# Kernel optimization log

Hardware: AMD Instinct MI355X
Metric: run time of the kernel (lower is better)

Reference implementation:

```python
import jax, jax.numpy as jnp
import numpy as np

K = 16  # top-k neighbors (init kwarg k)
EPS = 1e-8


def setup_inputs() -> dict:
    key = jax.random.key(0)
    # bs=8, closeness=12, flows=2, N=2048
    x_c = jax.random.normal(key, (8, 12, 2, 2048), dtype=jnp.float32)
    return {"x_c": x_c, "flow": 0}


def _cosine_adjacency(x):
    # x: (bs, 2, N, closeness) -> per-node feature = concat of both flows over time
    bs, f, N, c = x.shape
    feats = jnp.transpose(x, (0, 2, 1, 3)).reshape(bs, N, f * c)  # (bs, N, 2*closeness)
    fn = feats / (jnp.linalg.norm(feats, axis=-1, keepdims=True) + EPS)
    return jnp.einsum('bnd,bmd->bnm', fn, fn)  # (bs, N, N)


def reference(x_c, flow):
    # x_c: (bs, closeness, 2, N)
    bs, closeness, _, N = x_c.shape
    x = jnp.transpose(x_c, (0, 2, 3, 1)).astype(jnp.float32)  # (bs, 2, N, closeness)

    # mode == 'cos': cosine-similarity adjacency
    A = _cosine_adjacency(x)

    # index = argsort(A, descending)[:, :, :k]  ==  top-k neighbor indices per node
    _, index = jax.lax.top_k(A, K)  # (bs, N, K)

    # batched gather replacing the bs x N python double loop:
    # sx_c[i, j] = x[i, flow, index[i, j]]
    x_flow = x[:, flow]  # (bs, N, closeness)
    sx_c = jax.vmap(lambda xf, idx: xf[idx])(x_flow, index)  # (bs, N, K, closeness)

    # tgt_mode == 'c': tgt = x[:, flow].unsqueeze(-2)  -> (bs, N, 1, closeness)
    tgt = x_flow[:, :, None, :]
    # returned as tgt.permute(0,2,3,1).squeeze(1) -> (bs, closeness, N)
    tgt_out = jnp.squeeze(jnp.transpose(tgt, (0, 2, 3, 1)), axis=1)

    return sx_c, tgt_out
```

## Files before the change

kernel.cpp:

```cpp
#include <hip/hip_runtime.h>
#include <hip/hip_bf16.h>
#include <math.h>

#define BS   8
#define NPTS 2048
#define CCH  12
#define NF   2
#define DIM  24
#define KPAD 32
#define KTOP 16
#define NWV  8
#define RPB  16
#define CBUF 112
#define CBS  113
#define WVS  20

#define NROWS    (BS * NPTS)
#define TGT_BASE (NROWS * KTOP * CCH)

typedef unsigned long long u64;
typedef unsigned int       u32;
typedef unsigned short     u16;
typedef __attribute__((ext_vector_type(8))) short short8;
typedef __attribute__((ext_vector_type(4))) float f32x4;

#define WS_FEATS 0
#define WS_RAW   (NROWS * DIM * 4)
#define WS_FHI   (WS_RAW + NROWS * CCH * 4)
#define WS_FLO   (WS_FHI + NROWS * KPAD * 2)

__device__ __forceinline__ float np_norm_den(const float* __restrict__ v)
{
#pragma clang fp contract(off)
    float s[DIM];
    #pragma unroll
    for (int d = 0; d < DIM; ++d) s[d] = v[d] * v[d];
    float r[8];
    #pragma unroll
    for (int j = 0; j < 8; ++j) r[j] = (s[j] + s[j + 8]) + s[j + 16];
    float res = ((r[0] + r[1]) + (r[2] + r[3])) + ((r[4] + r[5]) + (r[6] + r[7]));
    return sqrtf(res) + 1e-8f;
}

__device__ __forceinline__ u32 ordf(float f)
{
    u32 u = __float_as_uint(f);
    return ((int)u >= 0) ? (u | 0x80000000u) : ~u;
}

__device__ __forceinline__ u16 bf16_rne(float x)
{
    u32 bits = __float_as_uint(x);
    bits += 0x7fffu + ((bits >> 16) & 1u);
    return (u16)(bits >> 16);
}

__global__ __launch_bounds__(64) void prep_kernel(
    const float* __restrict__ x_c,
    const int*   __restrict__ flow_p,
    float*       __restrict__ feats,
    u16*         __restrict__ fhi,
    u16*         __restrict__ flo,
    float*       __restrict__ raw,
    float*       __restrict__ out)
{
    const int t = blockIdx.x * 64 + threadIdx.x;
    const int b = t >> 11;
    const int n = t & (NPTS - 1);
    const float* xb = x_c + (size_t)b * CCH * NF * NPTS;

    float v[DIM];
    float fn[DIM];
    {
#pragma clang fp contract(off)
        #pragma unroll
        for (int c = 0; c < CCH; ++c)
            #pragma unroll
            for (int f = 0; f < NF; ++f)
                v[f * CCH + c] = xb[(c * NF + f) * NPTS + n];

        const float den = np_norm_den(v);
        #pragma unroll
        for (int d = 0; d < DIM; ++d) fn[d] = v[d] / den;
    }

    float* fo = feats + (size_t)t * DIM;
    #pragma unroll
    for (int j = 0; j < 6; ++j)
        *(f32x4*)(fo + 4 * j) = *(f32x4*)(fn + 4 * j);

    u16 hb[KPAD], lb[KPAD];
    #pragma unroll
    for (int d = 0; d < DIM; ++d) {
        const u16 h = bf16_rne(fn[d]);
        const float hf = __uint_as_float((u32)h << 16);
        hb[d] = h;
        lb[d] = bf16_rne(fn[d] - hf);
    }
    #pragma unroll
    for (int d = DIM; d < KPAD; ++d) { hb[d] = 0; lb[d] = 0; }

    u16* ho = fhi + (size_t)t * KPAD;
    u16* lo = flo + (size_t)t * KPAD;
    #pragma unroll
    for (int j = 0; j < 4; ++j) {
        *(short8*)(ho + 8 * j) = ((const short8*)hb)[j];
        *(short8*)(lo + 8 * j) = ((const short8*)lb)[j];
    }

    const int flow = flow_p[0];
    float rv[CCH];
    #pragma unroll
    for (int c = 0; c < CCH; ++c) {
        rv[c] = flow ? v[CCH + c] : v[c];
        out[TGT_BASE + ((size_t)b * CCH + c) * NPTS + n] = rv[c];
    }
    float* ro = raw + (size_t)t * CCH;
    #pragma unroll
    for (int j = 0; j < 3; ++j)
        *(f32x4*)(ro + 4 * j) = *(f32x4*)(rv + 4 * j);
}

#define CLEANUP_DESC(arr)                                         \
    _Pragma("unroll")                                             \
    for (int j_ = 8; j_ > 0; j_ >>= 1)                            \
        _Pragma("unroll")                                         \
        for (int i_ = 0; i_ < KTOP; ++i_) {                       \
            const int l_ = i_ | j_;                               \
            if (l_ > i_) {                                        \
                const float a_ = arr[i_], c_ = arr[l_];           \
                arr[i_] = fmaxf(a_, c_);                          \
                arr[l_] = fminf(a_, c_);                          \
            }                                                     \
        }

#define APPROX_TILE(ACC, AHI, ALO, BHI, BLO)                                  \
    f32x4 ACC  = {0.0f, 0.0f, 0.0f, 0.0f};                                    \
    {                                                                         \
        f32x4 acc2_ = {0.0f, 0.0f, 0.0f, 0.0f};                               \
        ACC   = __builtin_amdgcn_mfma_f32_16x16x32_bf16(AHI, BHI, ACC, 0,0,0);\
        acc2_ = __builtin_amdgcn_mfma_f32_16x16x32_bf16(AHI, BLO, acc2_,0,0,0);\
        ACC   = __builtin_amdgcn_mfma_f32_16x16x32_bf16(ALO, BHI, ACC, 0,0,0);\
        _Pragma("unroll")                                                     \
        for (int i_ = 0; i_ < 4; ++i_) ACC[i_] += acc2_[i_];                  \
    }

__global__ __launch_bounds__(512) void fused_topk_kernel(
    const float* __restrict__ feats,
    const u16*   __restrict__ fhi,
    const u16*   __restrict__ flo,
    const float* __restrict__ raw,
    float*       __restrict__ out)
{
    __shared__ union {
        float wval[NWV * 16 * WVS];
        float vk[NWV * KTOP * 16];
        u64   ckey[RPB * CBS];
    } sh;
    __shared__ float thr_s[RPB];
    __shared__ int   cnt[RPB];
    __shared__ int   sel[RPB][KTOP];

    const int tid  = threadIdx.x;
    const int lane = tid & 63;
    const int w    = __builtin_amdgcn_readfirstlane(tid >> 6);
    const int b     = blockIdx.x >> 7;
    const int chunk = blockIdx.x & 127;
    const int rb    = chunk * RPB;
    const int p     = lane & 15;
    const int q     = lane >> 4;

    if (tid < RPB) cnt[tid] = 0;

    short8 ahi, alo;
    {
        const size_t ae = ((size_t)(b * NPTS + rb + p)) * KPAD + q * 8;
        ahi = *(const short8*)(fhi + ae);
        alo = *(const short8*)(flo + ae);
    }

    float* wv = sh.wval + w * (16 * WVS);

    auto gather_sorted16 = [&](int ro, float bv[16]) {
        #pragma unroll
        for (int t = 0; t < 4; ++t) {
            const int cb0 = w * 128 + ro * 64 + t * 16;
            const size_t be = ((size_t)(b * NPTS + cb0 + p)) * KPAD + q * 8;
            const short8 bhi = *(const short8*)(fhi + be);
            const short8 blo = *(const short8*)(flo + be);
            APPROX_TILE(acc, ahi, alo, bhi, blo)
            *(f32x4*)(wv + p * WVS + q * 4) = acc;
            #pragma unroll
            for (int i = 0; i < 4; ++i)
                bv[t * 4 + i] = wv[(q * 4 + i) * WVS + p];
        }
        #pragma unroll
        for (int k = 2; k <= 16; k <<= 1)
            #pragma unroll
            for (int j = k >> 1; j > 0; j >>= 1)
                #pragma unroll
                for (int i = 0; i < 16; ++i) {
                    const int l = i | j;
                    if (l > i) {
                        const float a = bv[i], c = bv[l];
                        if ((i & k) == 0) { bv[i] = fminf(a, c); bv[l] = fmaxf(a, c); }
                        else              { bv[i] = fmaxf(a, c); bv[l] = fminf(a, c); }
                    }
                }
    };

    float vlist[KTOP];
    {
        float bv[16];
        gather_sorted16(0, bv);
        #pragma unroll
        for (int i = 0; i < 16; ++i) vlist[i] = bv[15 - i];
        gather_sorted16(1, bv);
        #pragma unroll
        for (int i = 0; i < 16; ++i) vlist[i] = fmaxf(vlist[i], bv[i]);
        CLEANUP_DESC(vlist)
    }

    #pragma unroll
    for (int x = 16; x <= 32; x <<= 1) {
        float other[KTOP];
        #pragma unroll
        for (int k = 0; k < KTOP; ++k) other[k] = __shfl_xor(vlist[k], x);
        #pragma unroll
        for (int i = 0; i < KTOP; ++i)
            vlist[i] = fmaxf(vlist[i], other[KTOP - 1 - i]);
        CLEANUP_DESC(vlist)
    }

    __syncthreads();

    if (q == 0) {
        #pragma unroll
        for (int k = 0; k < KTOP; ++k)
            sh.vk[(w * KTOP + k) * 16 + p] = vlist[k];
    }
    __syncthreads();
    if (w == 0) {
        float la[KTOP], lb[KTOP];
        #pragma unroll
        for (int k = 0; k < KTOP; ++k) {
            la[k] = sh.vk[(q * KTOP + k) * 16 + p];
            lb[k] = sh.vk[((q + 4) * KTOP + k) * 16 + p];
        }
        #pragma unroll
        for (int i = 0; i < KTOP; ++i)
            la[i] = fmaxf(la[i], lb[KTOP - 1 - i]);
        CLEANUP_DESC(la)
        #pragma unroll
        for (int x = 16; x <= 32; x <<= 1) {
            float other[KTOP];
            #pragma unroll
            for (int k = 0; k < KTOP; ++k) other[k] = __shfl_xor(la[k], x);
            #pragma unroll
            for (int i = 0; i < KTOP; ++i)
                la[i] = fmaxf(la[i], other[KTOP - 1 - i]);
            CLEANUP_DESC(la)
        }
        if (q == 0) thr_s[p] = la[KTOP - 1] - 8e-4f;
    }
    __syncthreads();

    float thrv[4];
    #pragma unroll
    for (int i = 0; i < 4; ++i) thrv[i] = thr_s[q * 4 + i];

    {
        size_t be_n = ((size_t)(b * NPTS + w * 256 + p)) * KPAD + q * 8;
        short8 nbhi = *(const short8*)(fhi + be_n);
        short8 nblo = *(const short8*)(flo + be_n);
        for (int t = 0; t < 16; ++t) {
            const int cb0 = w * 256 + t * 16;
            const short8 bhi = nbhi, blo = nblo;
            if (t < 15) {
                const size_t be = ((size_t)(b * NPTS + cb0 + 16 + p)) * KPAD + q * 8;
                nbhi = *(const short8*)(fhi + be);
                nblo = *(const short8*)(flo + be);
            }
            APPROX_TILE(acc, ahi, alo, bhi, blo)
            #pragma unroll
            for (int i = 0; i < 4; ++i) {
                if (acc[i] >= thrv[i]) {
                    const int r = q * 4 + i;
                    const int pos = atomicAdd(&cnt[r], 1);
                    if (pos < CBUF)
                        sh.ckey[r * CBS + pos] = (u64)(u32)(cb0 + p);
                }
            }
        }
    }
    __syncthreads();

    {
        const int r = tid & 15;
        const float* fr = feats + (size_t)(b * NPTS + rb + r) * DIM;
        float rfn[DIM];
        #pragma unroll
        for (int j = 0; j < 6; ++j)
            *(f32x4*)(rfn + 4 * j) = *(const f32x4*)(fr + 4 * j);
        const int e = (cnt[r] < CBUF) ? cnt[r] : CBUF;
        for (int pos = tid >> 4; pos < e; pos += 32) {
            const int idx = (int)(u32)sh.ckey[r * CBS + pos];
            const float* cp = feats + (size_t)(b * NPTS + idx) * DIM;
            float cv[DIM];
            #pragma unroll
            for (int j = 0; j < 6; ++j)
                *(f32x4*)(cv + 4 * j) = *(const f32x4*)(cp + 4 * j);
            float acc = 0.0f;
            #pragma unroll
            for (int d = 0; d < DIM; ++d)
                acc = __builtin_fmaf(cv[d], rfn[d], acc);
            sh.ckey[r * CBS + pos] = ((u64)ordf(acc) << 32) | (u32)(2047 - idx);
        }
    }
    __syncthreads();

    {
        const int L = tid >> 5;
        const int g = tid & 31;
        const int e = (cnt[L] < CBUF) ? cnt[L] : CBUF;
        const u64* rowbuf = &sh.ckey[L * CBS];
        for (int pos = g; pos < e; pos += 32) {
            const u64 key = rowbuf[pos];
            int rank = 0;
            for (int p2 = 0; p2 < e; ++p2) rank += (rowbuf[p2] > key);
            if (rank < KTOP) sel[L][rank] = 2047 - (int)(key & 0xFFFFFFFFull);
        }
    }
    __syncthreads();

    const int rg = b * NPTS + rb;
    for (int e2 = tid; e2 < RPB * KTOP * CCH; e2 += 512) {
        const int L = e2 / (KTOP * CCH);
        const int r = e2 % (KTOP * CCH);
        const int k = r / CCH;
        const int c = r % CCH;
        out[((size_t)(rg + L) * KTOP + k) * CCH + c] =
            raw[((size_t)b * NPTS + sel[L][k]) * CCH + c];
    }
}

extern "C" void kernel_launch(void* const* d_in, const int* in_sizes, int n_in,
                              void* d_out, int out_size, void* d_ws, size_t ws_size,
                              hipStream_t stream)
{
    const float* x_c    = (const float*)d_in[0];
    const int*   flow_p = (const int*)d_in[1];
    float*       out    = (float*)d_out;

    float* feats = (float*)((char*)d_ws + WS_FEATS);
    float* raw   = (float*)((char*)d_ws + WS_RAW);
    u16*   fhi   = (u16*)  ((char*)d_ws + WS_FHI);
    u16*   flo   = (u16*)  ((char*)d_ws + WS_FLO);

    prep_kernel<<<NROWS / 64, 64, 0, stream>>>(x_c, flow_p, feats, fhi, flo, raw, out);
    fused_topk_kernel<<<BS * 128, 512, 0, stream>>>(feats, fhi, flo, raw, out);
}
```

Measured before the change: 103.9 us.

## Use single bf16 MFMA screening with wider margin and top-4 sampled threshold

Drops the hi/lo split-bf16 product (three MFMAs per tile) and uses a single bf16 MFMA for candidate screening. It compensates for the lost precision with a larger threshold margin and a bigger candidate buffer. The threshold estimate now keeps a per-lane top-4 via med3 insertion instead of full 16-element bitonic sorts through LDS. Operands are swapped so each lane owns one row, which simplifies the atomics. The cost is more candidates per row for the exact fp32 rescoring stage, and a risk of buffer overflow or missed neighbours if the margin is too tight.

```diff
diff --git a/kernel.cpp b/kernel.cpp
--- a/kernel.cpp
+++ b/kernel.cpp
@@ -11,12 +11,13 @@
 #define KTOP 16
 #define NWV  8
 #define RPB  16
-#define CBUF 112
-#define CBS  113
-#define WVS  20
+#define CBUF 144
+#define CBS  145
 
 #define NROWS    (BS * NPTS)
 #define TGT_BASE (NROWS * KTOP * CCH)
+
+#define MARGIN 0.016f
 
 typedef unsigned long long u64;
 typedef unsigned int       u32;
@@ -27,7 +28,6 @@
 #define WS_FEATS 0
 #define WS_RAW   (NROWS * DIM * 4)
 #define WS_FHI   (WS_RAW + NROWS * CCH * 4)
-#define WS_FLO   (WS_FHI + NROWS * KPAD * 2)
 
 __device__ __forceinline__ float np_norm_den(const float* __restrict__ v)
 {
@@ -54,13 +54,30 @@
     bits += 0x7fffu + ((bits >> 16) & 1u);
     return (u16)(bits >> 16);
 }
+
+__device__ __forceinline__ void ins4(float& t0, float& t1, float& t2, float& t3, float v)
+{
+#if __has_builtin(__builtin_amdgcn_fmed3f)
+    const float n0 = fmaxf(t0, v);
+    const float n1 = __builtin_amdgcn_fmed3f(t0, t1, v);
+    const float n2 = __builtin_amdgcn_fmed3f(t1, t2, v);
+    const float n3 = __builtin_amdgcn_fmed3f(t2, t3, v);
+#else
+    const float n0 = fmaxf(t0, v);
+    const float n1 = fmaxf(t1, fminf(t0, v));
+    const float n2 = fmaxf(t2, fminf(t1, v));
+    const float n3 = fmaxf(t3, fminf(t2, v));
+#endif
+    t0 = n0; t1 = n1; t2 = n2; t3 = n3;
+}
+
+#define CE(a, b) { const float h_ = fmaxf(a, b), l_ = fminf(a, b); a = h_; b = l_; }
 
 __global__ __launch_bounds__(64) void prep_kernel(
     const float* __restrict__ x_c,
     const int*   __restrict__ flow_p,
     float*       __restrict__ feats,
     u16*         __restrict__ fhi,
-    u16*         __restrict__ flo,
     float*       __restrict__ raw,
     float*       __restrict__ out)
 {
@@ -89,24 +106,16 @@
     for (int j = 0; j < 6; ++j)
         *(f32x4*)(fo + 4 * j) = *(f32x4*)(fn + 4 * j);
 
-    u16 hb[KPAD], lb[KPAD];
-    #pragma unroll
-    for (int d = 0; d < DIM; ++d) {
-        const u16 h = bf16_rne(fn[d]);
-        const float hf = __uint_as_float((u32)h << 16);
-        hb[d] = h;
-        lb[d] = bf16_rne(fn[d] - hf);
-    }
-    #pragma unroll
-    for (int d = DIM; d < KPAD; ++d) { hb[d] = 0; lb[d] = 0; }
+    u16 hb[KPAD];
+    #pragma unroll
+    for (int d = 0; d < DIM; ++d) hb[d] = bf16_rne(fn[d]);
+    #pragma unroll
+    for (int d = DIM; d < KPAD; ++d) hb[d] = 0;
 
     u16* ho = fhi + (size_t)t * KPAD;
-    u16* lo = flo + (size_t)t * KPAD;
-    #pragma unroll
-    for (int j = 0; j < 4; ++j) {
+    #pragma unroll
+    for (int j = 0; j < 4; ++j)
         *(short8*)(ho + 8 * j) = ((const short8*)hb)[j];
-        *(short8*)(lo + 8 * j) = ((const short8*)lb)[j];
-    }
 
     const int flow = flow_p[0];
     float rv[CCH];
@@ -121,40 +130,14 @@
         *(f32x4*)(ro + 4 * j) = *(f32x4*)(rv + 4 * j);
 }
 
-#define CLEANUP_DESC(arr)                                         \
-    _Pragma("unroll")                                             \
-    for (int j_ = 8; j_ > 0; j_ >>= 1)                            \
-        _Pragma("unroll")                                         \
-        for (int i_ = 0; i_ < KTOP; ++i_) {                       \
-            const int l_ = i_ | j_;                               \
-            if (l_ > i_) {                                        \
-                const float a_ = arr[i_], c_ = arr[l_];           \
-                arr[i_] = fmaxf(a_, c_);                          \
-                arr[l_] = fminf(a_, c_);                          \
-            }                                                     \
-        }
-
-#define APPROX_TILE(ACC, AHI, ALO, BHI, BLO)                                  \
-    f32x4 ACC  = {0.0f, 0.0f, 0.0f, 0.0f};                                    \
-    {                                                                         \
-        f32x4 acc2_ = {0.0f, 0.0f, 0.0f, 0.0f};                               \
-        ACC   = __builtin_amdgcn_mfma_f32_16x16x32_bf16(AHI, BHI, ACC, 0,0,0);\
-        acc2_ = __builtin_amdgcn_mfma_f32_16x16x32_bf16(AHI, BLO, acc2_,0,0,0);\
-        ACC   = __builtin_amdgcn_mfma_f32_16x16x32_bf16(ALO, BHI, ACC, 0,0,0);\
-        _Pragma("unroll")                                                     \
-        for (int i_ = 0; i_ < 4; ++i_) ACC[i_] += acc2_[i_];                  \
-    }
-
 __global__ __launch_bounds__(512) void fused_topk_kernel(
     const float* __restrict__ feats,
     const u16*   __restrict__ fhi,
-    const u16*   __restrict__ flo,
     const float* __restrict__ raw,
     float*       __restrict__ out)
 {
     __shared__ union {
-        float wval[NWV * 16 * WVS];
-        float vk[NWV * KTOP * 16];
+        f32x4 vk4[NWV * 16];
         u64   ckey[RPB * CBS];
     } sh;
     __shared__ float thr_s[RPB];
@@ -172,123 +155,115 @@
 
     if (tid < RPB) cnt[tid] = 0;
 
-    short8 ahi, alo;
+    short8 arow;
     {
         const size_t ae = ((size_t)(b * NPTS + rb + p)) * KPAD + q * 8;
-        ahi = *(const short8*)(fhi + ae);
-        alo = *(const short8*)(flo + ae);
-    }
-
-    float* wv = sh.wval + w * (16 * WVS);
-
-    auto gather_sorted16 = [&](int ro, float bv[16]) {
-        #pragma unroll
-        for (int t = 0; t < 4; ++t) {
-            const int cb0 = w * 128 + ro * 64 + t * 16;
-            const size_t be = ((size_t)(b * NPTS + cb0 + p)) * KPAD + q * 8;
-            const short8 bhi = *(const short8*)(fhi + be);
-            const short8 blo = *(const short8*)(flo + be);
-            APPROX_TILE(acc, ahi, alo, bhi, blo)
-            *(f32x4*)(wv + p * WVS + q * 4) = acc;
-            #pragma unroll
-            for (int i = 0; i < 4; ++i)
-                bv[t * 4 + i] = wv[(q * 4 + i) * WVS + p];
-        }
-        #pragma unroll
-        for (int k = 2; k <= 16; k <<= 1)
-            #pragma unroll
-            for (int j = k >> 1; j > 0; j >>= 1)
+        arow = *(const short8*)(fhi + ae);
+    }
+
+    float ta0 = -3.0f, ta1 = -3.0f, ta2 = -3.0f, ta3 = -3.0f;
+    float tb0 = -3.0f, tb1 = -3.0f, tb2 = -3.0f, tb3 = -3.0f;
+    {
+        size_t be_n = ((size_t)(b * NPTS + w * 128 + p)) * KPAD + q * 8;
+        short8 nb = *(const short8*)(fhi + be_n);
+        #pragma unroll
+        for (int t = 0; t < 8; ++t) {
+            const short8 bh = nb;
+            if (t < 7) {
+                const size_t be = ((size_t)(b * NPTS + w * 128 + (t + 1) * 16 + p)) * KPAD + q * 8;
+                nb = *(const short8*)(fhi + be);
+            }
+            f32x4 acc = {0.0f, 0.0f, 0.0f, 0.0f};
+            acc = __builtin_amdgcn_mfma_f32_16x16x32_bf16(bh, arow, acc, 0, 0, 0);
+            if (t & 1) {
                 #pragma unroll
-                for (int i = 0; i < 16; ++i) {
-                    const int l = i | j;
-                    if (l > i) {
-                        const float a = bv[i], c = bv[l];
-                        if ((i & k) == 0) { bv[i] = fminf(a, c); bv[l] = fmaxf(a, c); }
-                        else              { bv[i] = fmaxf(a, c); bv[l] = fminf(a, c); }
-                    }
-                }
-    };
-
-    float vlist[KTOP];
-    {
-        float bv[16];
-        gather_sorted16(0, bv);
-        #pragma unroll
-        for (int i = 0; i < 16; ++i) vlist[i] = bv[15 - i];
-        gather_sorted16(1, bv);
-        #pragma unroll
-        for (int i = 0; i < 16; ++i) vlist[i] = fmaxf(vlist[i], bv[i]);
-        CLEANUP_DESC(vlist)
-    }
+                for (int i = 0; i < 4; ++i) ins4(tb0, tb1, tb2, tb3, acc[i]);
+            } else {
+                #pragma unroll
+                for (int i = 0; i < 4; ++i) ins4(ta0, ta1, ta2, ta3, acc[i]);
+            }
+        }
+    }
+    float t0 = fmaxf(ta0, tb3), t1 = fmaxf(ta1, tb2), t2 = fmaxf(ta2, tb1), t3 = fmaxf(ta3, tb0);
+    CE(t0, t2) CE(t1, t3) CE(t0, t1) CE(t2, t3)
 
     #pragma unroll
     for (int x = 16; x <= 32; x <<= 1) {
-        float other[KTOP];
-        #pragma unroll
-        for (int k = 0; k < KTOP; ++k) other[k] = __shfl_xor(vlist[k], x);
-        #pragma unroll
-        for (int i = 0; i < KTOP; ++i)
-            vlist[i] = fmaxf(vlist[i], other[KTOP - 1 - i]);
-        CLEANUP_DESC(vlist)
-    }
-
-    __syncthreads();
+        const float o0 = __shfl_xor(t0, x), o1 = __shfl_xor(t1, x);
+        const float o2 = __shfl_xor(t2, x), o3 = __shfl_xor(t3, x);
+        float m0 = fmaxf(t0, o3), m1 = fmaxf(t1, o2), m2 = fmaxf(t2, o1), m3 = fmaxf(t3, o0);
+        CE(m0, m2) CE(m1, m3) CE(m0, m1) CE(m2, m3)
+        t0 = m0; t1 = m1; t2 = m2; t3 = m3;
+    }
 
     if (q == 0) {
-        #pragma unroll
-        for (int k = 0; k < KTOP; ++k)
-            sh.vk[(w * KTOP + k) * 16 + p] = vlist[k];
-    }
-    __syncthreads();
+        f32x4 v4 = {t0, t1, t2, t3};
+        sh.vk4[w * 16 + p] = v4;
+    }
+    __syncthreads();
+
     if (w == 0) {
-        float la[KTOP], lb[KTOP];
-        #pragma unroll
-        for (int k = 0; k < KTOP; ++k) {
-            la[k] = sh.vk[(q * KTOP + k) * 16 + p];
-            lb[k] = sh.vk[((q + 4) * KTOP + k) * 16 + p];
-        }
-        #pragma unroll
-        for (int i = 0; i < KTOP; ++i)
-            la[i] = fmaxf(la[i], lb[KTOP - 1 - i]);
-        CLEANUP_DESC(la)
-        #pragma unroll
-        for (int x = 16; x <= 32; x <<= 1) {
-            float other[KTOP];
-            #pragma unroll
-            for (int k = 0; k < KTOP; ++k) other[k] = __shfl_xor(la[k], x);
-            #pragma unroll
-            for (int i = 0; i < KTOP; ++i)
-                la[i] = fmaxf(la[i], other[KTOP - 1 - i]);
-            CLEANUP_DESC(la)
-        }
-        if (q == 0) thr_s[p] = la[KTOP - 1] - 8e-4f;
-    }
-    __syncthreads();
-
-    float thrv[4];
-    #pragma unroll
-    for (int i = 0; i < 4; ++i) thrv[i] = thr_s[q * 4 + i];
+        const int j = q;
+        const f32x4 A  = sh.vk4[j * 16 + p];
+        const f32x4 Bv = sh.vk4[(j + 4) * 16 + p];
+        float s0 = fmaxf(A[0], Bv[3]), s1 = fmaxf(A[1], Bv[2]);
+        float s2 = fmaxf(A[2], Bv[1]), s3 = fmaxf(A[3], Bv[0]);
+        float s4 = fminf(A[0], Bv[3]), s5 = fminf(A[1], Bv[2]);
+        float s6 = fminf(A[2], Bv[1]), s7 = fminf(A[3], Bv[0]);
+        CE(s0, s2) CE(s1, s3) CE(s0, s1) CE(s2, s3)
+        CE(s4, s6) CE(s5, s7) CE(s4, s5) CE(s6, s7)
+        float s[8] = {s0, s1, s2, s3, s4, s5, s6, s7};
+        float t16[16];
+        {
+            float o[8];
+            #pragma unroll
+            for (int i = 0; i < 8; ++i) o[i] = __shfl_xor(s[i], 16);
+            #pragma unroll
+            for (int i = 0; i < 8; ++i) {
+                t16[i]     = fmaxf(s[i], o[7 - i]);
+                t16[8 + i] = fminf(s[i], o[7 - i]);
+            }
+            #pragma unroll
+            for (int base = 0; base < 16; base += 8) {
+                CE(t16[base + 0], t16[base + 4]) CE(t16[base + 1], t16[base + 5])
+                CE(t16[base + 2], t16[base + 6]) CE(t16[base + 3], t16[base + 7])
+                CE(t16[base + 0], t16[base + 2]) CE(t16[base + 1], t16[base + 3])
+                CE(t16[base + 4], t16[base + 6]) CE(t16[base + 5], t16[base + 7])
+                CE(t16[base + 0], t16[base + 1]) CE(t16[base + 2], t16[base + 3])
+                CE(t16[base + 4], t16[base + 5]) CE(t16[base + 6], t16[base + 7])
+            }
+        }
+        float z[16];
+        #pragma unroll
+        for (int i = 0; i < 16; ++i)
+            z[i] = fmaxf(t16[i], __shfl_xor(t16[15 - i], 32));
+        float mn = z[0];
+        #pragma unroll
+        for (int i = 1; i < 16; ++i) mn = fminf(mn, z[i]);
+        if (q == 0) thr_s[p] = mn - MARGIN;
+    }
+    __syncthreads();
+
+    const float thrp = thr_s[p];
 
     {
         size_t be_n = ((size_t)(b * NPTS + w * 256 + p)) * KPAD + q * 8;
-        short8 nbhi = *(const short8*)(fhi + be_n);
-        short8 nblo = *(const short8*)(flo + be_n);
+        short8 nb = *(const short8*)(fhi + be_n);
         for (int t = 0; t < 16; ++t) {
             const int cb0 = w * 256 + t * 16;
-            const short8 bhi = nbhi, blo = nblo;
+            const short8 bh = nb;
             if (t < 15) {
                 const size_t be = ((size_t)(b * NPTS + cb0 + 16 + p)) * KPAD + q * 8;
-                nbhi = *(const short8*)(fhi + be);
-                nblo = *(const short8*)(flo + be);
-            }
-            APPROX_TILE(acc, ahi, alo, bhi, blo)
+                nb = *(const short8*)(fhi + be);
+            }
+            f32x4 acc = {0.0f, 0.0f, 0.0f, 0.0f};
+            acc = __builtin_amdgcn_mfma_f32_16x16x32_bf16(bh, arow, acc, 0, 0, 0);
             #pragma unroll
             for (int i = 0; i < 4; ++i) {
-                if (acc[i] >= thrv[i]) {
-                    const int r = q * 4 + i;
-                    const int pos = atomicAdd(&cnt[r], 1);
+                if (acc[i] >= thrp) {
+                    const int pos = atomicAdd(&cnt[p], 1);
                     if (pos < CBUF)
-                        sh.ckey[r * CBS + pos] = (u64)(u32)(cb0 + p);
+                        sh.ckey[p * CBS + pos] = (u64)(u32)(cb0 + q * 4 + i);
                 }
             }
         }
@@ -355,8 +330,7 @@
     float* feats = (float*)((char*)d_ws + WS_FEATS);
     float* raw   = (float*)((char*)d_ws + WS_RAW);
     u16*   fhi   = (u16*)  ((char*)d_ws + WS_FHI);
-    u16*   flo   = (u16*)  ((char*)d_ws + WS_FLO);
-
-    prep_kernel<<<NROWS / 64, 64, 0, stream>>>(x_c, flow_p, feats, fhi, flo, raw, out);
-    fused_topk_kernel<<<BS * 128, 512, 0, stream>>>(feats, fhi, flo, raw, out);
-}
+
+    prep_kernel<<<NROWS / 64, 64, 0, stream>>>(x_c, flow_p, feats, fhi, raw, out);
+    fused_topk_kernel<<<BS * 128, 512, 0, stream>>>(feats, fhi, raw, out);
+}
```

New measurement: 93.34 us. 1.11x faster.
